# Kernel optimization log

Measured on AMD Instinct MI355X. Metric: run time of the kernel, lower is better.

## Reference

```python
import jax, jax.numpy as jnp
import numpy as np

HEADS = 4
DIM_HEAD = 32
EPS = 1e-5


def setup_inputs() -> dict:
    key = jax.random.key(0)
    ks = jax.random.split(key, 4)
    B, dim, H, W = 8, 256, 128, 128
    hidden = HEADS * DIM_HEAD  # 128
    x = jax.random.normal(ks[0], (B, dim, H, W), dtype=jnp.float32)
    # 1x1 conv weights stored as [out_ch, in_ch]
    qkv_w = jax.random.normal(ks[1], (3 * hidden, dim), dtype=jnp.float32) * (1.0 / np.sqrt(dim))
    conv_w = jax.random.normal(ks[2], (dim, hidden), dtype=jnp.float32) * (1.0 / np.sqrt(hidden))
    conv_b = jax.random.normal(ks[3], (dim,), dtype=jnp.float32) * 0.01
    gamma = jnp.ones((dim,), dtype=jnp.float32)
    beta = jnp.zeros((dim,), dtype=jnp.float32)
    return {"x": x, "qkv_w": qkv_w, "conv_w": conv_w, "conv_b": conv_b,
            "gamma": gamma, "beta": beta}


def reference(x, qkv_w, conv_w, conv_b, gamma, beta):
    B, C, H, W = x.shape
    N = H * W
    scale = DIM_HEAD ** (-0.5)
    # qkv 1x1 conv -> [B, 3, heads, dim_head, N]
    qkv = jnp.einsum('oc,bchw->bohw', qkv_w, x).reshape(B, 3, HEADS, DIM_HEAD, N)
    q, k, v = qkv[:, 0], qkv[:, 1], qkv[:, 2]
    q = jax.nn.softmax(q, axis=-2) * scale   # softmax over dim_head axis
    k = jax.nn.softmax(k, axis=-1)           # softmax over spatial axis
    v = v / N
    # context = k @ v^T : [B, h, d, d]
    context = jnp.einsum('bhdn,bhen->bhde', k, v)
    # out = context @ q : [B, h, d, N]
    out = jnp.einsum('bhde,bhen->bhdn', context, q)
    out = out.reshape(B, HEADS * DIM_HEAD, H, W)
    # final 1x1 conv with bias
    y = jnp.einsum('oc,bchw->bohw', conv_w, out) + conv_b[None, :, None, None]
    # InstanceNorm2d(affine=True): per-sample per-channel over (H, W), biased var
    mean = jnp.mean(y, axis=(2, 3), keepdims=True)
    var = jnp.var(y, axis=(2, 3), keepdims=True)
    y = (y - mean) * jax.lax.rsqrt(var + EPS)
    return y * gamma[None, :, None, None] + beta[None, :, None, None]
```

## Files before the change

kernel.cpp:

```cpp
#include <hip/hip_runtime.h>
#include <math.h>

#define NPIX 16384
#define DIMC 256
#define BATCH 8
#define HEADS 4
#define DHEAD 32
#define HID 128
#define OQKV 384
#define EPS 1e-5f
#define SCALE 0.17677669529663687f

typedef _Float16 f16x8 __attribute__((ext_vector_type(8)));
typedef float f32x4 __attribute__((ext_vector_type(4)));

__device__ inline void gl_lds16(const void* g, void* l) {
    __builtin_amdgcn_global_load_lds(
        (const __attribute__((address_space(1))) unsigned*)g,
        (__attribute__((address_space(3))) unsigned*)l, 16, 0, 0);
}

__global__ __launch_bounds__(256) void prep_kernel(
    const float* __restrict__ qkv_w, const float* __restrict__ conv_w,
    _Float16* __restrict__ wh, _Float16* __restrict__ ch, float* __restrict__ zbuf)
{
    int i = blockIdx.x * 256 + threadIdx.x;
    if (i < 98304) wh[i] = (_Float16)qkv_w[i];
    else           ch[i - 98304] = (_Float16)conv_w[i - 98304];
    if (i < 37888) zbuf[i] = 0.f;
}

__global__ __launch_bounds__(256) void gemm_qkv(
    const _Float16* __restrict__ A,
    const float* __restrict__ X,
    _Float16* __restrict__ Cm)
{
    __shared__ _Float16 smem[16384];
    _Float16* As = smem;
    float* Xs = (float*)(smem + 4096);
    const int t  = threadIdx.x;
    const int b  = blockIdx.x;
    const int m0 = blockIdx.y * 128;
    const int n0 = blockIdx.z * 128;
    const float* Xb = X + (long)b * DIMC * NPIX;
    const int w = t >> 6, lane = t & 63;
    const int q = lane >> 4, l16 = lane & 15;
    const int mw = (w >> 1) * 64, nw = (w & 1) * 64;
    const int swzq = ((q & 1) << 4) | ((q >> 1) << 2);

    f32x4 acc[4][4] = {};

    for (int k0 = 0; k0 < DIMC; k0 += 32) {
        #pragma unroll
        for (int is = 0; is < 2; is++) {
            int idx = is * 256 + t;
            int row = idx >> 2, kc = (idx & 3) * 8;
            gl_lds16(&A[(long)(m0 + row) * DIMC + k0 + kc], &As[idx * 8]);
        }
        #pragma unroll
        for (int is = 0; is < 4; is++) {
            int idx = is * 256 + t;
            int c = idx >> 5, f4 = (idx & 31) * 4;
            int qc = c >> 3;
            int sw = ((qc & 1) << 4) | ((qc >> 1) << 2);
            gl_lds16(&Xb[(long)(k0 + c) * NPIX + n0 + (f4 ^ sw)], &Xs[c * 128 + f4]);
        }
        __syncthreads();
        f16x8 af[4], bf[4];
        #pragma unroll
        for (int i = 0; i < 4; i++)
            af[i] = *(const f16x8*)&As[(mw + i * 16 + l16) * 32 + q * 8];
        #pragma unroll
        for (int i = 0; i < 4; i++) {
            int n = nw + i * 16 + l16;
            const float* xp = &Xs[q * 8 * 128 + (n ^ swzq)];
            #pragma unroll
            for (int j = 0; j < 8; j++) bf[i][j] = (_Float16)xp[j * 128];
        }
        #pragma unroll
        for (int i = 0; i < 4; i++)
            #pragma unroll
            for (int j = 0; j < 4; j++)
                acc[i][j] = __builtin_amdgcn_mfma_f32_16x16x32_f16(af[i], bf[j], acc[i][j], 0, 0, 0);
        __syncthreads();
    }

    _Float16* Cs = smem;
    #pragma unroll
    for (int i = 0; i < 4; i++) {
        #pragma unroll
        for (int j = 0; j < 4; j++) {
            #pragma unroll
            for (int r = 0; r < 4; r++) {
                int row = mw + i * 16 + q * 4 + r;
                int col = nw + j * 16 + l16;
                Cs[row * 128 + (col ^ ((row & 15) << 3))] = (_Float16)acc[i][j][r];
            }
        }
    }
    __syncthreads();
    _Float16* Cb = Cm + (long)b * ((long)OQKV * NPIX);
    #pragma unroll
    for (int it = 0; it < 8; it++) {
        int u = it * 256 + t;
        int row = u >> 4, cg = u & 15;
        f16x8 v8 = *(const f16x8*)&Cs[row * 128 + ((cg * 8) ^ ((row & 15) << 3))];
        *(f16x8*)&Cb[(long)(m0 + row) * NPIX + n0 + cg * 8] = v8;
    }
}

template<int K, int EPI>
__global__ __launch_bounds__(256) void gemm_h(
    const _Float16* __restrict__ A,
    const _Float16* __restrict__ Bm,
    _Float16* __restrict__ Cm,
    long bsB, long bsC, float* __restrict__ lnacc)
{
    __shared__ _Float16 smem[16384];
    _Float16* As = smem;
    _Float16* Bs = smem + 4096;
    const int t  = threadIdx.x;
    const int b  = blockIdx.x;
    const int m0 = blockIdx.y * 128;
    const int n0 = blockIdx.z * 128;
    const _Float16* Bb = Bm + (long)b * bsB;
    const int w = t >> 6, lane = t & 63;
    const int q = lane >> 4, l16 = lane & 15;
    const int mw = (w >> 1) * 64, nw = (w & 1) * 64;

    f32x4 acc[4][4] = {};

    for (int k0 = 0; k0 < K; k0 += 32) {
        #pragma unroll
        for (int is = 0; is < 2; is++) {
            int idx = is * 256 + t;
            int row = idx >> 2, kc = (idx & 3) * 8;
            gl_lds16(&A [(long)(m0 + row) * K + k0 + kc], &As[idx * 8]);
            gl_lds16(&Bb[(long)(n0 + row) * K + k0 + kc], &Bs[idx * 8]);
        }
        __syncthreads();
        f16x8 af[4], bf[4];
        #pragma unroll
        for (int i = 0; i < 4; i++) {
            af[i] = *(const f16x8*)&As[(mw + i * 16 + l16) * 32 + q * 8];
            bf[i] = *(const f16x8*)&Bs[(nw + i * 16 + l16) * 32 + q * 8];
        }
        #pragma unroll
        for (int i = 0; i < 4; i++)
            #pragma unroll
            for (int j = 0; j < 4; j++)
                acc[i][j] = __builtin_amdgcn_mfma_f32_16x16x32_f16(af[i], bf[j], acc[i][j], 0, 0, 0);
        __syncthreads();
    }

    _Float16* Cs = smem;
    #pragma unroll
    for (int i = 0; i < 4; i++) {
        #pragma unroll
        for (int j = 0; j < 4; j++) {
            #pragma unroll
            for (int r = 0; r < 4; r++) {
                int row = mw + i * 16 + q * 4 + r;
                int col = nw + j * 16 + l16;
                Cs[row * 128 + (col ^ ((row & 15) << 3))] = (_Float16)acc[i][j][r];
            }
        }
    }
    __syncthreads();
    _Float16* Cb = Cm + (long)b * bsC;
    #pragma unroll
    for (int it = 0; it < 8; it++) {
        int u = it * 256 + t;
        int row = u >> 4, cg = u & 15;
        f16x8 v8 = *(const f16x8*)&Cs[row * 128 + ((cg * 8) ^ ((row & 15) << 3))];
        *(f16x8*)&Cb[(long)(m0 + row) * NPIX + n0 + cg * 8] = v8;
        if (EPI) {
            float s = 0.f, sq = 0.f;
            #pragma unroll
            for (int k = 0; k < 8; k++) { float f = (float)v8[k]; s += f; sq += f * f; }
            #pragma unroll
            for (int off = 8; off > 0; off >>= 1) {
                s  += __shfl_down(s,  off, 16);
                sq += __shfl_down(sq, off, 16);
            }
            if ((t & 15) == 0) {
                int rg = b * DIMC + m0 + row;
                atomicAdd(&lnacc[rg * 2],     s);
                atomicAdd(&lnacc[rg * 2 + 1], sq);
            }
        }
    }
}

__global__ __launch_bounds__(256) void ctx_mfma(const _Float16* __restrict__ qkvh,
    float* __restrict__ ctx_raw, float* __restrict__ ksum)
{
    __shared__ float cbuf[4][1024];
    int t = threadIdx.x;
    int w = t >> 6, lane = t & 63;
    int q = lane >> 4, l16 = lane & 15;
    int bh = blockIdx.y, b = bh >> 2, h = bh & 3;
    const _Float16* kb = qkvh + ((long)b * OQKV + HID + h * DHEAD) * NPIX;
    const _Float16* vb = qkvh + ((long)b * OQKV + 2 * HID + h * DHEAD) * NPIX;
    long n0 = (long)blockIdx.x * 2048 + w * 512 + q * 8;

    f32x4 c00 = {}, c01 = {}, c10 = {}, c11 = {};
    float ks0 = 0.f, ks1 = 0.f;

    for (int s = 0; s < 16; s++) {
        long n = n0 + s * 32;
        f16x8 kf0 = *(const f16x8*)&kb[(long)l16 * NPIX + n];
        f16x8 kf1 = *(const f16x8*)&kb[(long)(16 + l16) * NPIX + n];
        f16x8 vf0 = *(const f16x8*)&vb[(long)l16 * NPIX + n];
        f16x8 vf1 = *(const f16x8*)&vb[(long)(16 + l16) * NPIX + n];
        f16x8 e0, e1;
        #pragma unroll
        for (int j = 0; j < 8; j++) {
            float ea = __expf((float)kf0[j]); e0[j] = (_Float16)ea; ks0 += ea;
            float eb = __expf((float)kf1[j]); e1[j] = (_Float16)eb; ks1 += eb;
        }
        c00 = __builtin_amdgcn_mfma_f32_16x16x32_f16(e0, vf0, c00, 0, 0, 0);
        c01 = __builtin_amdgcn_mfma_f32_16x16x32_f16(e0, vf1, c01, 0, 0, 0);
        c10 = __builtin_amdgcn_mfma_f32_16x16x32_f16(e1, vf0, c10, 0, 0, 0);
        c11 = __builtin_amdgcn_mfma_f32_16x16x32_f16(e1, vf1, c11, 0, 0, 0);
    }

    ks0 += __shfl_down(ks0, 32); ks0 += __shfl_down(ks0, 16);
    ks1 += __shfl_down(ks1, 32); ks1 += __shfl_down(ks1, 16);
    if (lane < 16) {
        atomicAdd(&ksum[bh * DHEAD + l16],      ks0);
        atomicAdd(&ksum[bh * DHEAD + 16 + l16], ks1);
    }

    float* cb = cbuf[w];
    #pragma unroll
    for (int r = 0; r < 4; r++) {
        cb[(q * 4 + r) * 32 + l16]            = c00[r];
        cb[(q * 4 + r) * 32 + 16 + l16]       = c01[r];
        cb[(16 + q * 4 + r) * 32 + l16]       = c10[r];
        cb[(16 + q * 4 + r) * 32 + 16 + l16]  = c11[r];
    }
    __syncthreads();
    #pragma unroll
    for (int ii = 0; ii < 4; ii++) {
        int idx = ii * 256 + t;
        float s = cbuf[0][idx] + cbuf[1][idx] + cbuf[2][idx] + cbuf[3][idx];
        atomicAdd(&ctx_raw[(long)bh * 1024 + idx], s);
    }
}

__global__ __launch_bounds__(256) void outq_h(_Float16* __restrict__ qkvh,
    const float* __restrict__ ctx_raw, const float* __restrict__ ksum)
{
    __shared__ float ctx_t[4][32][32];
    int tid = threadIdx.x;
    int n = blockIdx.x * 256 + tid;
    int b = blockIdx.y;
    #pragma unroll
    for (int i = 0; i < 16; i++) {
        int idx = i * 256 + tid;
        int h = idx >> 10, de = idx & 1023;
        int d = de >> 5, e = de & 31;
        float s = ksum[(b * 4 + h) * DHEAD + d];
        ctx_t[h][e][d] = SCALE * ctx_raw[(long)(b * 4 + h) * 1024 + de] / s;
    }
    __syncthreads();
    _Float16* ob = qkvh + ((long)b * OQKV + 2 * HID) * NPIX + (long)n * HID;
    for (int h = 0; h < 4; h++) {
        const _Float16* qb = qkvh + ((long)b * OQKV + h * DHEAD) * NPIX + n;
        float qv[32];
        float mx = -1e30f;
        #pragma unroll
        for (int e = 0; e < 32; e++) { qv[e] = (float)qb[(long)e * NPIX]; mx = fmaxf(mx, qv[e]); }
        float s = 0.f;
        #pragma unroll
        for (int e = 0; e < 32; e++) { qv[e] = __expf(qv[e] - mx); s += qv[e]; }
        float qs = 1.f / s;
        float4 o4[8];
        #pragma unroll
        for (int j = 0; j < 8; j++) o4[j] = make_float4(0,0,0,0);
        #pragma unroll 8
        for (int e = 0; e < 32; e++) {
            float qe = qv[e] * qs;
            #pragma unroll
            for (int j = 0; j < 8; j++) {
                float4 c = *(const float4*)&ctx_t[h][e][j * 4];
                o4[j].x += c.x * qe; o4[j].y += c.y * qe;
                o4[j].z += c.z * qe; o4[j].w += c.w * qe;
            }
        }
        #pragma unroll
        for (int j = 0; j < 4; j++) {
            f16x8 pk;
            float4 a = o4[j * 2], bb = o4[j * 2 + 1];
            pk[0] = (_Float16)a.x;  pk[1] = (_Float16)a.y;
            pk[2] = (_Float16)a.z;  pk[3] = (_Float16)a.w;
            pk[4] = (_Float16)bb.x; pk[5] = (_Float16)bb.y;
            pk[6] = (_Float16)bb.z; pk[7] = (_Float16)bb.w;
            *(f16x8*)&ob[h * DHEAD + j * 8] = pk;
        }
    }
}

__global__ __launch_bounds__(256) void ln_finalize(const float* __restrict__ lnacc,
    const float* __restrict__ gamma, const float* __restrict__ beta,
    float* __restrict__ mv)
{
    int row = blockIdx.x * 256 + threadIdx.x;
    float s = lnacc[row * 2], sq = lnacc[row * 2 + 1];
    float meanp = s * (1.f / NPIX);
    float varp  = fmaxf(sq * (1.f / NPIX) - meanp * meanp, 0.f);
    float rinv  = rsqrtf(varp * (1.f / ((float)NPIX * (float)NPIX)) + EPS);
    int c = row & 255;
    float g = rinv * gamma[c];
    mv[row * 2]     = g * (1.f / NPIX);
    mv[row * 2 + 1] = beta[c] - meanp * (1.f / NPIX) * g;
}

__global__ __launch_bounds__(256) void ln_apply(const _Float16* __restrict__ yh,
    const float* __restrict__ mv, float* __restrict__ out)
{
    long i8 = (long)blockIdx.x * 256 + threadIdx.x;
    int row = (int)(i8 >> 11);
    float a = mv[row * 2], be = mv[row * 2 + 1];
    f16x8 v = *(const f16x8*)&yh[i8 * 8];
    float4 o1, o2;
    o1.x = (float)v[0] * a + be; o1.y = (float)v[1] * a + be;
    o1.z = (float)v[2] * a + be; o1.w = (float)v[3] * a + be;
    o2.x = (float)v[4] * a + be; o2.y = (float)v[5] * a + be;
    o2.z = (float)v[6] * a + be; o2.w = (float)v[7] * a + be;
    *(float4*)&out[i8 * 8]     = o1;
    *(float4*)&out[i8 * 8 + 4] = o2;
}

extern "C" void kernel_launch(void* const* d_in, const int* in_sizes, int n_in,
                              void* d_out, int out_size, void* d_ws, size_t ws_size,
                              hipStream_t stream)
{
    const float* x      = (const float*)d_in[0];
    const float* qkv_w  = (const float*)d_in[1];
    const float* conv_w = (const float*)d_in[2];
    const float* gamma  = (const float*)d_in[4];
    const float* beta   = (const float*)d_in[5];
    float* out = (float*)d_out;

    _Float16* yh   = (_Float16*)d_ws;
    _Float16* qkvh = yh + 33554432;
    _Float16* wh   = qkvh + 50331648;
    _Float16* ch   = wh + 98304;
    float* ctx_raw = (float*)(ch + 32768);
    float* ksum    = ctx_raw + 32768;
    float* lnacc   = ksum + 1024;
    float* mv      = lnacc + 4096;

    prep_kernel<<<512, 256, 0, stream>>>(qkv_w, conv_w, wh, ch, ctx_raw);
    gemm_qkv<<<dim3(BATCH, 3, 128), 256, 0, stream>>>(wh, x, qkvh);
    ctx_mfma<<<dim3(8, 32), 256, 0, stream>>>(qkvh, ctx_raw, ksum);
    outq_h<<<dim3(64, BATCH), 256, 0, stream>>>(qkvh, ctx_raw, ksum);
    gemm_h<128, 1><<<dim3(BATCH, 2, 128), 256, 0, stream>>>(
        ch, qkvh + (long)2 * HID * NPIX, yh, (long)OQKV * NPIX, (long)DIMC * NPIX, lnacc);
    ln_finalize<<<8, 256, 0, stream>>>(lnacc, gamma, beta, mv);
    ln_apply<<<16384, 256, 0, stream>>>(yh, mv, out);
}
```

Baseline: 377.4 us.

## Double-buffer QKV GEMM tiles and vectorize LDS reads with permuted column mapping

The QKV projection GEMM now uses two LDS stages so the next K-slice's async global-to-LDS loads are issued before computing on the current slice, with one barrier per iteration. The X operand is loaded unswizzled and read as float4 per lane, with the N columns assigned to lanes in a permuted order. The epilogue writes packed 4-wide half vectors to match that order. This doubles LDS use, which may reduce occupancy, and relies on the barrier waiting for the async loads.

```diff
diff --git a/kernel.cpp b/kernel.cpp
--- a/kernel.cpp
+++ b/kernel.cpp
@@ -12,6 +12,7 @@
 #define SCALE 0.17677669529663687f
 
 typedef _Float16 f16x8 __attribute__((ext_vector_type(8)));
+typedef _Float16 f16x4 __attribute__((ext_vector_type(4)));
 typedef float f32x4 __attribute__((ext_vector_type(4)));
 
 __device__ inline void gl_lds16(const void* g, void* l) {
@@ -35,9 +36,7 @@
     const float* __restrict__ X,
     _Float16* __restrict__ Cm)
 {
-    __shared__ _Float16 smem[16384];
-    _Float16* As = smem;
-    float* Xs = (float*)(smem + 4096);
+    __shared__ _Float16 smem[24576];
     const int t  = threadIdx.x;
     const int b  = blockIdx.x;
     const int m0 = blockIdx.y * 128;
@@ -46,11 +45,12 @@
     const int w = t >> 6, lane = t & 63;
     const int q = lane >> 4, l16 = lane & 15;
     const int mw = (w >> 1) * 64, nw = (w & 1) * 64;
-    const int swzq = ((q & 1) << 4) | ((q >> 1) << 2);
 
     f32x4 acc[4][4] = {};
 
-    for (int k0 = 0; k0 < DIMC; k0 += 32) {
+    auto STAGE = [&](int buf, int k0) {
+        _Float16* As = smem + buf * 12288;
+        float*    Xs = (float*)(smem + buf * 12288 + 4096);
         #pragma unroll
         for (int is = 0; is < 2; is++) {
             int idx = is * 256 + t;
@@ -61,41 +61,55 @@
         for (int is = 0; is < 4; is++) {
             int idx = is * 256 + t;
             int c = idx >> 5, f4 = (idx & 31) * 4;
-            int qc = c >> 3;
-            int sw = ((qc & 1) << 4) | ((qc >> 1) << 2);
-            gl_lds16(&Xb[(long)(k0 + c) * NPIX + n0 + (f4 ^ sw)], &Xs[c * 128 + f4]);
-        }
-        __syncthreads();
+            gl_lds16(&Xb[(long)(k0 + c) * NPIX + n0 + f4], &Xs[c * 128 + f4]);
+        }
+    };
+
+    STAGE(0, 0);
+    __syncthreads();
+    int cur = 0;
+
+    for (int kt = 0; kt < 8; kt++) {
+        if (kt < 7) STAGE(cur ^ 1, (kt + 1) * 32);
+
+        const _Float16* As = smem + cur * 12288;
+        const float*    Xs = (const float*)(smem + cur * 12288 + 4096);
+
         f16x8 af[4], bf[4];
         #pragma unroll
         for (int i = 0; i < 4; i++)
             af[i] = *(const f16x8*)&As[(mw + i * 16 + l16) * 32 + q * 8];
         #pragma unroll
-        for (int i = 0; i < 4; i++) {
-            int n = nw + i * 16 + l16;
-            const float* xp = &Xs[q * 8 * 128 + (n ^ swzq)];
-            #pragma unroll
-            for (int j = 0; j < 8; j++) bf[i][j] = (_Float16)xp[j * 128];
+        for (int kk = 0; kk < 8; kk++) {
+            f32x4 xv = *(const f32x4*)&Xs[(q * 8 + kk) * 128 + nw + l16 * 4];
+            bf[0][kk] = (_Float16)xv[0];
+            bf[1][kk] = (_Float16)xv[1];
+            bf[2][kk] = (_Float16)xv[2];
+            bf[3][kk] = (_Float16)xv[3];
         }
         #pragma unroll
         for (int i = 0; i < 4; i++)
             #pragma unroll
             for (int j = 0; j < 4; j++)
                 acc[i][j] = __builtin_amdgcn_mfma_f32_16x16x32_f16(af[i], bf[j], acc[i][j], 0, 0, 0);
+
         __syncthreads();
+        cur ^= 1;
     }
 
     _Float16* Cs = smem;
     #pragma unroll
     for (int i = 0; i < 4; i++) {
         #pragma unroll
-        for (int j = 0; j < 4; j++) {
-            #pragma unroll
-            for (int r = 0; r < 4; r++) {
-                int row = mw + i * 16 + q * 4 + r;
-                int col = nw + j * 16 + l16;
-                Cs[row * 128 + (col ^ ((row & 15) << 3))] = (_Float16)acc[i][j][r];
-            }
+        for (int r = 0; r < 4; r++) {
+            int row = mw + i * 16 + q * 4 + r;
+            int col = nw + l16 * 4;
+            f16x4 h4;
+            h4[0] = (_Float16)acc[i][0][r];
+            h4[1] = (_Float16)acc[i][1][r];
+            h4[2] = (_Float16)acc[i][2][r];
+            h4[3] = (_Float16)acc[i][3][r];
+            *(f16x4*)&Cs[row * 128 + (col ^ ((row & 15) << 3))] = h4;
         }
     }
     __syncthreads();
```

Result: no change. 374.9 us (-0.7%).
